# Kernel optimization log

Measured on AMD Instinct MI355X. Metric: run time of the kernel, lower is better.

## Reference

```python
import jax, jax.numpy as jnp
import numpy as np

BIT_WIDTH = 1
LEVELS = 2 ** BIT_WIDTH - 1
# Floyd-Steinberg gather weights (mirrored scatter kernel): contributions to
# pixel (r,c) from (r-1,c-1), (r-1,c), (r-1,c+1), (r,c-1)
W_UL, W_U, W_UR, W_L = 1.0 / 16, 5.0 / 16, 3.0 / 16, 7.0 / 16


def quant(x):
    return jnp.round(x * LEVELS) / LEVELS


def dither(x01):
    """Raster-scan error-diffusion dithering. x01: [B,C,R,W] in [0,1]."""
    B, C, R, W = x01.shape
    dtype = x01.dtype

    def row_step(prev_err, row_x):
        # prev_err: [B,C,W+2] zero-padded errors of previous row
        # row_x:    [W,B,C]   input values of current row
        up = (W_UL * prev_err[..., 0:W]
              + W_U * prev_err[..., 1:W + 1]
              + W_UR * prev_err[..., 2:W + 2])          # [B,C,W]
        up = jnp.moveaxis(up, -1, 0)                     # [W,B,C]

        def col_step(left_err, xs):
            x, u = xs                                    # each [B,C]
            val = jnp.clip(x + u + W_L * left_err, 0.0, 1.0)
            err = val - quant(val)
            return err, (val, err)

        _, (vals, errs) = jax.lax.scan(col_step, jnp.zeros((B, C), dtype), (row_x, up))
        err_row = jnp.pad(jnp.moveaxis(errs, 0, -1), ((0, 0), (0, 0), (1, 1)))  # [B,C,W+2]
        return err_row, jnp.moveaxis(vals, 0, -1)        # carry, [B,C,W]

    rows_x = jnp.moveaxis(jnp.moveaxis(x01, 2, 0), -1, 1)  # [R,W,B,C]
    init = jnp.zeros((B, C, W + 2), dtype)
    _, out_rows = jax.lax.scan(row_step, init, rows_x)      # [R,B,C,W]
    out = jnp.moveaxis(out_rows, 0, 2)                      # [B,C,R,W]
    return quant(out)


def setup_inputs() -> dict:
    key = jax.random.key(0)
    x = jax.random.normal(key, (32, 3, 512, 512), dtype=jnp.float32)
    return {"x": x}


def reference(x):
    x = jnp.clip(x, -1.0, 1.0)
    x01 = (x + 1.0) / 2.0
    y = dither(x01)
    return y * 2.0 - 1.0
```

## Files before the change

### kernel.cpp

```cpp
#include <hip/hip_runtime.h>


#define F_UL 0.0625f
#define F_U  0.3125f
#define F_UR 0.1875f
#define F_L  0.4375f

constexpr int WW    = 512;
constexpr int IMG   = WW * WW;
constexpr int NIMG  = 96;
constexpr int NW    = 8;
constexpr int BUFW  = 792;
constexpr int NCH   = 40;
constexpr int LAG   = 10;
constexpr int PPAIR = 320;
constexpr size_t XP_FLOATS = (size_t)NIMG * NW * PPAIR * 128;
constexpr size_t XP_BYTES  = XP_FLOATS * 4;
constexpr size_t XP_SLACK  = 8192;
constexpr size_t XP_OFF    = 4u * 1024 * 1024;
constexpr size_t WS_NEED   = XP_OFF + XP_BYTES + XP_SLACK;

__device__ __forceinline__ float wave_shr1(float v, float fill) {
  int r = __builtin_amdgcn_update_dpp(__float_as_int(fill), __float_as_int(v),
                                      0x138 , 0xF, 0xF, false);
  return __int_as_float(r);
}

__device__ __forceinline__ float pp(float xv) {
#pragma clang fp contract(off)
  float xc = fminf(fmaxf(xv, -1.0f), 1.0f);
  return (xc + 1.0f) * 0.5f;
}

__global__ __launch_bounds__(256)
void pack_kernel(const float* __restrict__ xin, float* __restrict__ xp) {
  __shared__ float tile[64 * 65];
  const int img = blockIdx.x, w = blockIdx.y, ct = blockIdx.z;
  const int C   = ct * 64;
  const int tid = threadIdx.x;

  const float* xg = xin + (size_t)img * IMG + (size_t)w * 64 * WW;
  for (int k = 0; k < 4; ++k) {
    int flat = tid + 256 * k;
    int row = flat >> 4, cq = flat & 15;
    float4 v = *(const float4*)(xg + row * WW + C + cq * 4);
    float* d = tile + row * 65 + cq * 4;
    d[0] = pp(v.x); d[1] = pp(v.y); d[2] = pp(v.z); d[3] = pp(v.w);
  }
  __syncthreads();

  float* ob = xp + ((size_t)(img * NW + w) * PPAIR + 32 * ct) * 128;
  const int l = tid & 63, mo = tid >> 6;
  const int kst = (l - mo + 3) >> 2;
  for (int k = 0; k < 8; ++k) {
    int m = mo + 4 * (kst + k);
    if (m <= 94) {
      int c = 2 * (m - l);
      float2 v = make_float2(tile[l * 65 + c], tile[l * 65 + c + 1]);
      *(float2*)(ob + (size_t)m * 128 + 2 * l) = v;
    }
  }
}

__global__ __launch_bounds__(512, 1)
void dither_packed(const float* __restrict__ xp, uint2* __restrict__ yb) {
  __shared__ float bnd[(NW + 1) * BUFW];
  __shared__ int flags[NW];

  const int  tid  = threadIdx.x;
  const int  wave = tid >> 6;
  const int  lane = tid & 63;
  const int  img  = blockIdx.x;
  const bool l63  = (lane == 63);

  for (int i = tid; i < (NW + 1) * BUFW; i += 512) bnd[i] = 0.0f;
  if (tid < NW) flags[tid] = 0;
  __syncthreads();

  uint2* ybw = yb + (size_t)(img * NW + wave) * (10 * 64);
  const float* xw = xp + ((size_t)(img * NW + wave) * PPAIR) * 128 + lane * 2;
  float* bufR = bnd + wave * BUFW;
  float* bufW = bnd + (wave + 1) * BUFW;
  const int c0 = -2 * lane;

  float2 A0 = *(const float2*)(xw + 0 * 128);
  float2 A1 = *(const float2*)(xw + 1 * 128);
  float2 A2 = *(const float2*)(xw + 2 * 128);
  float2 A3 = *(const float2*)(xw + 3 * 128);
  float2 m0 = *(const float2*)(xw + 4 * 128);
  float2 m1 = *(const float2*)(xw + 5 * 128);
  float2 m2 = *(const float2*)(xw + 6 * 128);
  float2 m3 = *(const float2*)(xw + 7 * 128);
  float2 f0 = *(const float2*)(xw + 8 * 128);
  float2 f1 = *(const float2*)(xw + 9 * 128);
  float2 f2 = *(const float2*)(xw + 10 * 128);
  float2 f3 = *(const float2*)(xw + 11 * 128);
  float2 g0 = *(const float2*)(xw + 12 * 128);
  float2 g1 = *(const float2*)(xw + 13 * 128);
  float2 g2 = *(const float2*)(xw + 14 * 128);
  float2 g3 = *(const float2*)(xw + 15 * 128);
  float xq0 = A0.x, xq1 = A0.y, xq2 = A1.x, xq3 = A1.y;
  float xq4 = A2.x, xq5 = A2.y, xq6 = A3.x, xq7 = A3.y;

  if (wave) {
    while (__hip_atomic_load(&flags[wave - 1], __ATOMIC_RELAXED,
                             __HIP_MEMORY_SCOPE_WORKGROUP) < LAG)
      __builtin_amdgcn_s_sleep(1);
    __asm__ volatile("s_waitcnt lgkmcnt(0)" ::: "memory");
  }

  float err = 0.0f, s2 = 0.0f;
  float s1 = (lane == 0) ? bufR[129] : 0.0f;
  float2 qa = *(const float2*)(bufR + 130);
  float2 qb = *(const float2*)(bufR + 132);
  float2 qc = *(const float2*)(bufR + 134);
  float2 qd = *(const float2*)(bufR + 136);
  float2 fa = *(const float2*)(bufR + 138);
  float2 fb = *(const float2*)(bufR + 140);
  float2 fc = *(const float2*)(bufR + 142);
  float2 fd = *(const float2*)(bufR + 144);

  unsigned accLo = 0u, accHi = 0u;

  auto step = [&](int c, float qv, float xv) -> float {
#pragma clang fp contract(off)
    float e_in = wave_shr1(err, qv);
    float t1   = F_UL * s2;
    float t2   = F_U  * s1;
    float t3   = F_UR * e_in;
    float u    = (t1 + t2) + t3;
    float a1   = xv + u;
    float b    = F_L * err;
    float v    = a1 + b;
    float val  = fminf(fmaxf(v, 0.0f), 1.0f);
    float qn   = rintf(val);
    float e    = val - qn;
    float en   = ((unsigned)c < 512u) ? e : 0.0f;
    err = en; s2 = s1; s1 = e_in;
    return qn;
  };

  auto iter8 = [&](int T, unsigned& acc) {
    const int cg  = c0 + T;
    const int bsh = T & 31;
    const float* lp = xw + (size_t)(T / 2 + 16) * 128;
    float2 n0 = *(const float2*)(lp + 0 * 128);
    float2 n1 = *(const float2*)(lp + 1 * 128);
    float2 n2 = *(const float2*)(lp + 2 * 128);
    float2 n3 = *(const float2*)(lp + 3 * 128);
    float2 h0 = *(const float2*)(bufR + (T + 146));
    float2 h1 = *(const float2*)(bufR + (T + 148));
    float2 h2 = *(const float2*)(bufR + (T + 150));
    float2 h3 = *(const float2*)(bufR + (T + 152));

    float p0 = step(cg + 0, qa.x, xq0); float e0 = err;
    float p1 = step(cg + 1, qa.y, xq1); float e1 = err;
    float p2 = step(cg + 2, qb.x, xq2); float e2 = err;
    float p3 = step(cg + 3, qb.y, xq3); float e3 = err;
    float p4 = step(cg + 4, qc.x, xq4); float e4 = err;
    float p5 = step(cg + 5, qc.y, xq5); float e5 = err;
    float p6 = step(cg + 6, qd.x, xq6); float e6 = err;
    float p7 = step(cg + 7, qd.y, xq7); float e7 = err;

    acc |= ((__float_as_uint(p0) >> 29) & 1u) << (bsh + 0);
    acc |= ((__float_as_uint(p1) >> 29) & 1u) << (bsh + 1);
    acc |= ((__float_as_uint(p2) >> 29) & 1u) << (bsh + 2);
    acc |= ((__float_as_uint(p3) >> 29) & 1u) << (bsh + 3);
    acc |= ((__float_as_uint(p4) >> 29) & 1u) << (bsh + 4);
    acc |= ((__float_as_uint(p5) >> 29) & 1u) << (bsh + 5);
    acc |= ((__float_as_uint(p6) >> 29) & 1u) << (bsh + 6);
    acc |= ((__float_as_uint(p7) >> 29) & 1u) << (bsh + 7);

    if (l63) {
      float* bw = bufW + (cg + 129);
      bw[0] = e0; bw[1] = e1; bw[2] = e2; bw[3] = e3;
      bw[4] = e4; bw[5] = e5; bw[6] = e6; bw[7] = e7;
    }

    xq0 = m0.x; xq1 = m0.y; xq2 = m1.x; xq3 = m1.y;
    xq4 = m2.x; xq5 = m2.y; xq6 = m3.x; xq7 = m3.y;
    m0 = f0; m1 = f1; m2 = f2; m3 = f3;
    f0 = g0; f1 = g1; f2 = g2; f3 = g3;
    g0 = n0; g1 = n1; g2 = n2; g3 = n3;
    qa = fa; qb = fb; qc = fc; qd = fd;
    fa = h0; fb = h1; fc = h2; fd = h3;
  };

  for (int j = 0; j < NCH; ++j) {
    if (wave) {
      int need = j + LAG; if (need > NCH) need = NCH;
      while (__hip_atomic_load(&flags[wave - 1], __ATOMIC_RELAXED,
                               __HIP_MEMORY_SCOPE_WORKGROUP) < need)
        __builtin_amdgcn_s_sleep(1);
      __asm__ volatile("s_waitcnt lgkmcnt(0)" ::: "memory");
    }
    if (j & 2) { iter8(16 * j, accHi); iter8(16 * j + 8, accHi); }
    else       { iter8(16 * j, accLo); iter8(16 * j + 8, accLo); }
    if ((j & 3) == 3) {
      ybw[(j >> 2) * 64 + lane] = make_uint2(accLo, accHi);
      accLo = 0u; accHi = 0u;
    }
    if (l63) {
      __asm__ volatile("s_waitcnt lgkmcnt(0)" ::: "memory");
      __hip_atomic_store(&flags[wave], j + 1, __ATOMIC_RELAXED,
                         __HIP_MEMORY_SCOPE_WORKGROUP);
    }
  }
}

__global__ __launch_bounds__(256)
void unpack_kernel(const unsigned long long* __restrict__ yb,
                   float* __restrict__ yout) {
  const int img = blockIdx.x, w = blockIdx.y;
  const int wv = threadIdx.x >> 6, lane = threadIdx.x & 63;
  const unsigned long long* ybr = yb + (size_t)(img * NW + w) * 640;
  float* yb0 = yout + (size_t)img * IMG + (size_t)w * 64 * WW;

  for (int rr = 0; rr < 16; ++rr) {
    const int r  = wv * 16 + rr;
    const int t0 = 8 * lane + 2 * r;
    const int t64 = t0 >> 6, sh = t0 & 63;
    unsigned long long w1 = ybr[(size_t)t64 * 64 + r];
    unsigned long long w2 = ybr[(size_t)(t64 + 1) * 64 + r];
    unsigned bits = (unsigned)((w1 >> sh) | ((w2 << 1) << (63 - sh)));
    float* orow = yb0 + (size_t)r * WW + 8 * lane;
    float4 v0, v1;
    v0.x = (bits & 1u)   ? 1.0f : -1.0f;
    v0.y = (bits & 2u)   ? 1.0f : -1.0f;
    v0.z = (bits & 4u)   ? 1.0f : -1.0f;
    v0.w = (bits & 8u)   ? 1.0f : -1.0f;
    v1.x = (bits & 16u)  ? 1.0f : -1.0f;
    v1.y = (bits & 32u)  ? 1.0f : -1.0f;
    v1.z = (bits & 64u)  ? 1.0f : -1.0f;
    v1.w = (bits & 128u) ? 1.0f : -1.0f;
    *(float4*)(orow)     = v0;
    *(float4*)(orow + 4) = v1;
  }
}

__global__ __launch_bounds__(512, 1)
void dither_direct(const float* __restrict__ xin, float* __restrict__ yout) {
  __shared__ float bnd[(NW + 1) * BUFW];
  __shared__ int flags[NW];

  const int  tid  = threadIdx.x;
  const int  wave = tid >> 6;
  const int  lane = tid & 63;
  const int  img  = blockIdx.x;
  const bool l63  = (lane == 63);

  for (int i = tid; i < (NW + 1) * BUFW; i += 512) bnd[i] = 0.0f;
  if (tid < NW) flags[tid] = 0;
  __syncthreads();

  const int r = wave * 64 + lane;
  const float* xrow = xin + (size_t)img * IMG + (size_t)r * WW;
  float*       yrow = yout + (size_t)img * IMG + (size_t)r * WW;
  float* bufR = bnd + wave * BUFW;
  float* bufW = bnd + (wave + 1) * BUFW;
  const int c0 = -2 * lane;

  auto ldx = [&](int c) -> float2 { return *(const float2*)(xrow + (c & 511)); };

  float2 A0 = ldx(c0 + 0),  A1 = ldx(c0 + 2),  A2 = ldx(c0 + 4),  A3 = ldx(c0 + 6);
  float2 pB0 = ldx(c0 + 8),  pB1 = ldx(c0 + 10), pB2 = ldx(c0 + 12), pB3 = ldx(c0 + 14);
  float2 pC0 = ldx(c0 + 16), pC1 = ldx(c0 + 18), pC2 = ldx(c0 + 20), pC3 = ldx(c0 + 22);
  float xq0 = pp(A0.x), xq1 = pp(A0.y), xq2 = pp(A1.x), xq3 = pp(A1.y);
  float xq4 = pp(A2.x), xq5 = pp(A2.y), xq6 = pp(A3.x), xq7 = pp(A3.y);
  float2 pA0 = pB0, pA1 = pB1, pA2 = pB2, pA3 = pB3;
  pB0 = pC0; pB1 = pC1; pB2 = pC2; pB3 = pC3;

  if (wave) {
    while (__hip_atomic_load(&flags[wave - 1], __ATOMIC_RELAXED,
                             __HIP_MEMORY_SCOPE_WORKGROUP) < LAG)
      __builtin_amdgcn_s_sleep(1);
    __asm__ volatile("s_waitcnt lgkmcnt(0)" ::: "memory");
  }

  float err = 0.0f, s2 = 0.0f;
  float s1 = (lane == 0) ? bufR[129] : 0.0f;
  float2 qa = *(const float2*)(bufR + 130);
  float2 qb = *(const float2*)(bufR + 132);
  float2 qc = *(const float2*)(bufR + 134);
  float2 qd = *(const float2*)(bufR + 136);
  float2 fa = *(const float2*)(bufR + 138);
  float2 fb = *(const float2*)(bufR + 140);
  float2 fc = *(const float2*)(bufR + 142);
  float2 fd = *(const float2*)(bufR + 144);

  auto step = [&](int c, float qv, float xv) -> float {
#pragma clang fp contract(off)
    float e_in = wave_shr1(err, qv);
    float t1   = F_UL * s2;
    float t2   = F_U  * s1;
    float t3   = F_UR * e_in;
    float u    = (t1 + t2) + t3;
    float a1   = xv + u;
    float b    = F_L * err;
    float v    = a1 + b;
    float val  = fminf(fmaxf(v, 0.0f), 1.0f);
    float qn   = rintf(val);
    float e    = val - qn;
    float en   = ((unsigned)c < 512u) ? e : 0.0f;
    err = en; s2 = s1; s1 = e_in;
    return __builtin_fmaf(qn, 2.0f, -1.0f);
  };

  auto iter8 = [&](int T) {
    const int cg = c0 + T;
    float2 n0 = ldx(cg + 24), n1 = ldx(cg + 26), n2 = ldx(cg + 28), n3 = ldx(cg + 30);
    float2 h0 = *(const float2*)(bufR + (T + 146));
    float2 h1 = *(const float2*)(bufR + (T + 148));
    float2 h2 = *(const float2*)(bufR + (T + 150));
    float2 h3 = *(const float2*)(bufR + (T + 152));
    float w0 = pp(pA0.x), w1 = pp(pA0.y), w2 = pp(pA1.x), w3 = pp(pA1.y);
    float w4 = pp(pA2.x), w5 = pp(pA2.y), w6 = pp(pA3.x), w7 = pp(pA3.y);

    float y0 = step(cg + 0, qa.x, xq0); float e0 = err;
    float y1 = step(cg + 1, qa.y, xq1); float e1 = err;
    float y2 = step(cg + 2, qb.x, xq2); float e2 = err;
    float y3 = step(cg + 3, qb.y, xq3); float e3 = err;
    float y4 = step(cg + 4, qc.x, xq4); float e4 = err;
    float y5 = step(cg + 5, qc.y, xq5); float e5 = err;
    float y6 = step(cg + 6, qd.x, xq6); float e6 = err;
    float y7 = step(cg + 7, qd.y, xq7); float e7 = err;

    if ((unsigned)(cg + 0) < 511u) *(float2*)(yrow + cg + 0) = make_float2(y0, y1);
    if ((unsigned)(cg + 2) < 511u) *(float2*)(yrow + cg + 2) = make_float2(y2, y3);
    if ((unsigned)(cg + 4) < 511u) *(float2*)(yrow + cg + 4) = make_float2(y4, y5);
    if ((unsigned)(cg + 6) < 511u) *(float2*)(yrow + cg + 6) = make_float2(y6, y7);

    if (l63) {
      float* bw = bufW + (cg + 129);
      bw[0] = e0; bw[1] = e1; bw[2] = e2; bw[3] = e3;
      bw[4] = e4; bw[5] = e5; bw[6] = e6; bw[7] = e7;
    }

    xq0 = w0; xq1 = w1; xq2 = w2; xq3 = w3;
    xq4 = w4; xq5 = w5; xq6 = w6; xq7 = w7;
    pA0 = pB0; pA1 = pB1; pA2 = pB2; pA3 = pB3;
    pB0 = n0;  pB1 = n1;  pB2 = n2;  pB3 = n3;
    qa = fa; qb = fb; qc = fc; qd = fd;
    fa = h0; fb = h1; fc = h2; fd = h3;
  };

  for (int j = 0; j < NCH; ++j) {
    if (wave) {
      int need = j + LAG; if (need > NCH) need = NCH;
      while (__hip_atomic_load(&flags[wave - 1], __ATOMIC_RELAXED,
                               __HIP_MEMORY_SCOPE_WORKGROUP) < need)
        __builtin_amdgcn_s_sleep(1);
      __asm__ volatile("s_waitcnt lgkmcnt(0)" ::: "memory");
    }
    iter8(16 * j);
    iter8(16 * j + 8);
    if (l63) {
      __asm__ volatile("s_waitcnt lgkmcnt(0)" ::: "memory");
      __hip_atomic_store(&flags[wave], j + 1, __ATOMIC_RELAXED,
                         __HIP_MEMORY_SCOPE_WORKGROUP);
    }
  }
}

extern "C" void kernel_launch(void* const* d_in, const int* in_sizes, int n_in,
                              void* d_out, int out_size, void* d_ws, size_t ws_size,
                              hipStream_t stream) {
  const float* x = (const float*)d_in[0];
  float*       y = (float*)d_out;
  if (ws_size >= WS_NEED) {
    unsigned long long* yb = (unsigned long long*)d_ws;
    float* xp = (float*)((char*)d_ws + XP_OFF);
    pack_kernel<<<dim3(NIMG, NW, 8), dim3(256), 0, stream>>>(x, xp);
    dither_packed<<<dim3(NIMG), dim3(512), 0, stream>>>(xp, (uint2*)yb);
    unpack_kernel<<<dim3(NIMG, NW), dim3(256), 0, stream>>>(yb, y);
  } else {
    dither_direct<<<dim3(NIMG), dim3(512), 0, stream>>>(x, y);
  }
}
```

Before: 328.7 us.

## Pad out-of-range pixels with sentinel in pack, drop column bounds check in dither

The pack kernel now runs one block per image strip and walks column tiles through a 4-deep shared ring. It writes a -8 sentinel for out-of-range diagonal positions, so the dither step clamps these to zero error and can drop its per-step column bounds select. The dither loop is unrolled by four chunks with rotating register arrays, which replaces the long register shift chains. It also caches the last-seen flag value to skip redundant LDS polls and uses fmed3 for the clamp. The risks are less parallelism in pack (a smaller grid with serialized tiles) and a correctness dependence on the sentinel producing exactly zero error.

Result: faster. 282.6 us (-14.0%).

```diff
diff --git a/kernel.cpp b/kernel.cpp
--- a/kernel.cpp
+++ b/kernel.cpp
@@ -34,31 +34,44 @@
 
 __global__ __launch_bounds__(256)
 void pack_kernel(const float* __restrict__ xin, float* __restrict__ xp) {
-  __shared__ float tile[64 * 65];
-  const int img = blockIdx.x, w = blockIdx.y, ct = blockIdx.z;
-  const int C   = ct * 64;
+  __shared__ float ring[4 * 4160];
+  const int img = blockIdx.x, w = blockIdx.y;
   const int tid = threadIdx.x;
+  const int wv  = tid >> 6, l = tid & 63;
 
   const float* xg = xin + (size_t)img * IMG + (size_t)w * 64 * WW;
-  for (int k = 0; k < 4; ++k) {
-    int flat = tid + 256 * k;
-    int row = flat >> 4, cq = flat & 15;
-    float4 v = *(const float4*)(xg + row * WW + C + cq * 4);
-    float* d = tile + row * 65 + cq * 4;
-    d[0] = pp(v.x); d[1] = pp(v.y); d[2] = pp(v.z); d[3] = pp(v.w);
-  }
+  float* ob = xp + ((size_t)(img * NW + w) * PPAIR) * 128;
+
+  auto load_tile = [&](int t) {
+    float* dst = ring + (t & 3) * 4160;
+    const float* src = xg + 64 * t;
+#pragma unroll
+    for (int k = 0; k < 4; ++k) {
+      int flat = tid + 256 * k;
+      int row = flat >> 4, cq = flat & 15;
+      float4 v = *(const float4*)(src + row * WW + cq * 4);
+      float* d = dst + row * 65 + cq * 4;
+      d[0] = pp(v.x); d[1] = pp(v.y); d[2] = pp(v.z); d[3] = pp(v.w);
+    }
+  };
+
+  load_tile(0);
   __syncthreads();
-
-  float* ob = xp + ((size_t)(img * NW + w) * PPAIR + 32 * ct) * 128;
-  const int l = tid & 63, mo = tid >> 6;
-  const int kst = (l - mo + 3) >> 2;
-  for (int k = 0; k < 8; ++k) {
-    int m = mo + 4 * (kst + k);
-    if (m <= 94) {
-      int c = 2 * (m - l);
-      float2 v = make_float2(tile[l * 65 + c], tile[l * 65 + c + 1]);
-      *(float2*)(ob + (size_t)m * 128 + 2 * l) = v;
-    }
+  for (int t = 0; t < 10; ++t) {
+    if (t < 7) load_tile(t + 1);
+    const int Mb = 32 * t + 8 * wv;
+#pragma unroll
+    for (int i = 0; i < 8; ++i) {
+      const int M  = Mb + i;
+      const int g  = 2 * (M - l);
+      const int gm = g & 511;
+      const int idx = ((gm >> 6) & 3) * 4160 + l * 65 + (gm & 63);
+      const bool ok = ((unsigned)g < 512u);
+      float va = ring[idx], vb = ring[idx + 1];
+      float2 v = make_float2(ok ? va : -8.0f, ok ? vb : -8.0f);
+      *(float2*)(ob + (size_t)M * 128 + 2 * l) = v;
+    }
+    __syncthreads();
   }
 }
 
@@ -81,48 +94,36 @@
   const float* xw = xp + ((size_t)(img * NW + wave) * PPAIR) * 128 + lane * 2;
   float* bufR = bnd + wave * BUFW;
   float* bufW = bnd + (wave + 1) * BUFW;
-  const int c0 = -2 * lane;
-
-  float2 A0 = *(const float2*)(xw + 0 * 128);
-  float2 A1 = *(const float2*)(xw + 1 * 128);
-  float2 A2 = *(const float2*)(xw + 2 * 128);
-  float2 A3 = *(const float2*)(xw + 3 * 128);
-  float2 m0 = *(const float2*)(xw + 4 * 128);
-  float2 m1 = *(const float2*)(xw + 5 * 128);
-  float2 m2 = *(const float2*)(xw + 6 * 128);
-  float2 m3 = *(const float2*)(xw + 7 * 128);
-  float2 f0 = *(const float2*)(xw + 8 * 128);
-  float2 f1 = *(const float2*)(xw + 9 * 128);
-  float2 f2 = *(const float2*)(xw + 10 * 128);
-  float2 f3 = *(const float2*)(xw + 11 * 128);
-  float2 g0 = *(const float2*)(xw + 12 * 128);
-  float2 g1 = *(const float2*)(xw + 13 * 128);
-  float2 g2 = *(const float2*)(xw + 14 * 128);
-  float2 g3 = *(const float2*)(xw + 15 * 128);
-  float xq0 = A0.x, xq1 = A0.y, xq2 = A1.x, xq3 = A1.y;
-  float xq4 = A2.x, xq5 = A2.y, xq6 = A3.x, xq7 = A3.y;
-
+
+  float2 X0[4], X1[4], X2[4], X3[4], X4[4], X5[4], X6[4], X7[4];
+#pragma unroll
+  for (int i = 0; i < 4; ++i) {
+    X0[i] = *(const float2*)(xw + (size_t)(0  + i) * 128);
+    X1[i] = *(const float2*)(xw + (size_t)(4  + i) * 128);
+    X2[i] = *(const float2*)(xw + (size_t)(8  + i) * 128);
+    X3[i] = *(const float2*)(xw + (size_t)(12 + i) * 128);
+  }
+
+  int seen = 0;
   if (wave) {
-    while (__hip_atomic_load(&flags[wave - 1], __ATOMIC_RELAXED,
-                             __HIP_MEMORY_SCOPE_WORKGROUP) < LAG)
+    while ((seen = __hip_atomic_load(&flags[wave - 1], __ATOMIC_RELAXED,
+                                     __HIP_MEMORY_SCOPE_WORKGROUP)) < LAG)
       __builtin_amdgcn_s_sleep(1);
     __asm__ volatile("s_waitcnt lgkmcnt(0)" ::: "memory");
   }
 
   float err = 0.0f, s2 = 0.0f;
   float s1 = (lane == 0) ? bufR[129] : 0.0f;
-  float2 qa = *(const float2*)(bufR + 130);
-  float2 qb = *(const float2*)(bufR + 132);
-  float2 qc = *(const float2*)(bufR + 134);
-  float2 qd = *(const float2*)(bufR + 136);
-  float2 fa = *(const float2*)(bufR + 138);
-  float2 fb = *(const float2*)(bufR + 140);
-  float2 fc = *(const float2*)(bufR + 142);
-  float2 fd = *(const float2*)(bufR + 144);
+  float2 Q0[4], Q1[4];
+#pragma unroll
+  for (int i = 0; i < 4; ++i) {
+    Q0[i] = *(const float2*)(bufR + 130 + 2 * i);
+    Q1[i] = *(const float2*)(bufR + 138 + 2 * i);
+  }
 
   unsigned accLo = 0u, accHi = 0u;
 
-  auto step = [&](int c, float qv, float xv) -> float {
+  auto step = [&](float qv, float xv) -> float {
 #pragma clang fp contract(off)
     float e_in = wave_shr1(err, qv);
     float t1   = F_UL * s2;
@@ -132,35 +133,34 @@
     float a1   = xv + u;
     float b    = F_L * err;
     float v    = a1 + b;
-    float val  = fminf(fmaxf(v, 0.0f), 1.0f);
+    float val  = __builtin_amdgcn_fmed3f(v, 0.0f, 1.0f);
     float qn   = rintf(val);
-    float e    = val - qn;
-    float en   = ((unsigned)c < 512u) ? e : 0.0f;
-    err = en; s2 = s1; s1 = e_in;
+    err = val - qn;
+    s2 = s1; s1 = e_in;
     return qn;
   };
 
-  auto iter8 = [&](int T, unsigned& acc) {
-    const int cg  = c0 + T;
-    const int bsh = T & 31;
+  auto iter8 = [&](float2 (&XC)[4], float2 (&XL)[4], float2 (&QC)[4],
+                   int T, int bsh, unsigned& acc) {
     const float* lp = xw + (size_t)(T / 2 + 16) * 128;
-    float2 n0 = *(const float2*)(lp + 0 * 128);
-    float2 n1 = *(const float2*)(lp + 1 * 128);
-    float2 n2 = *(const float2*)(lp + 2 * 128);
-    float2 n3 = *(const float2*)(lp + 3 * 128);
-    float2 h0 = *(const float2*)(bufR + (T + 146));
-    float2 h1 = *(const float2*)(bufR + (T + 148));
-    float2 h2 = *(const float2*)(bufR + (T + 150));
-    float2 h3 = *(const float2*)(bufR + (T + 152));
-
-    float p0 = step(cg + 0, qa.x, xq0); float e0 = err;
-    float p1 = step(cg + 1, qa.y, xq1); float e1 = err;
-    float p2 = step(cg + 2, qb.x, xq2); float e2 = err;
-    float p3 = step(cg + 3, qb.y, xq3); float e3 = err;
-    float p4 = step(cg + 4, qc.x, xq4); float e4 = err;
-    float p5 = step(cg + 5, qc.y, xq5); float e5 = err;
-    float p6 = step(cg + 6, qd.x, xq6); float e6 = err;
-    float p7 = step(cg + 7, qd.y, xq7); float e7 = err;
+    XL[0] = *(const float2*)(lp + 0 * 128);
+    XL[1] = *(const float2*)(lp + 1 * 128);
+    XL[2] = *(const float2*)(lp + 2 * 128);
+    XL[3] = *(const float2*)(lp + 3 * 128);
+
+    float p0 = step(QC[0].x, XC[0].x); float e0 = err;
+    float p1 = step(QC[0].y, XC[0].y); float e1 = err;
+    float p2 = step(QC[1].x, XC[1].x); float e2 = err;
+    float p3 = step(QC[1].y, XC[1].y); float e3 = err;
+    float p4 = step(QC[2].x, XC[2].x); float e4 = err;
+    float p5 = step(QC[2].y, XC[2].y); float e5 = err;
+    float p6 = step(QC[3].x, XC[3].x); float e6 = err;
+    float p7 = step(QC[3].y, XC[3].y); float e7 = err;
+
+    QC[0] = *(const float2*)(bufR + (T + 146));
+    QC[1] = *(const float2*)(bufR + (T + 148));
+    QC[2] = *(const float2*)(bufR + (T + 150));
+    QC[3] = *(const float2*)(bufR + (T + 152));
 
     acc |= ((__float_as_uint(p0) >> 29) & 1u) << (bsh + 0);
     acc |= ((__float_as_uint(p1) >> 29) & 1u) << (bsh + 1);
@@ -172,39 +172,51 @@
     acc |= ((__float_as_uint(p7) >> 29) & 1u) << (bsh + 7);
 
     if (l63) {
-      float* bw = bufW + (cg + 129);
+      float* bw = bufW + (T + 3);
       bw[0] = e0; bw[1] = e1; bw[2] = e2; bw[3] = e3;
       bw[4] = e4; bw[5] = e5; bw[6] = e6; bw[7] = e7;
     }
-
-    xq0 = m0.x; xq1 = m0.y; xq2 = m1.x; xq3 = m1.y;
-    xq4 = m2.x; xq5 = m2.y; xq6 = m3.x; xq7 = m3.y;
-    m0 = f0; m1 = f1; m2 = f2; m3 = f3;
-    f0 = g0; f1 = g1; f2 = g2; f3 = g3;
-    g0 = n0; g1 = n1; g2 = n2; g3 = n3;
-    qa = fa; qb = fb; qc = fc; qd = fd;
-    fa = h0; fb = h1; fc = h2; fd = h3;
-  };
-
-  for (int j = 0; j < NCH; ++j) {
+  };
+
+  auto waitflag = [&](int j) {
     if (wave) {
       int need = j + LAG; if (need > NCH) need = NCH;
-      while (__hip_atomic_load(&flags[wave - 1], __ATOMIC_RELAXED,
-                               __HIP_MEMORY_SCOPE_WORKGROUP) < need)
-        __builtin_amdgcn_s_sleep(1);
-      __asm__ volatile("s_waitcnt lgkmcnt(0)" ::: "memory");
-    }
-    if (j & 2) { iter8(16 * j, accHi); iter8(16 * j + 8, accHi); }
-    else       { iter8(16 * j, accLo); iter8(16 * j + 8, accLo); }
-    if ((j & 3) == 3) {
-      ybw[(j >> 2) * 64 + lane] = make_uint2(accLo, accHi);
-      accLo = 0u; accHi = 0u;
-    }
+      if (seen < need) {
+        while ((seen = __hip_atomic_load(&flags[wave - 1], __ATOMIC_RELAXED,
+                                         __HIP_MEMORY_SCOPE_WORKGROUP)) < need)
+          __builtin_amdgcn_s_sleep(1);
+        __asm__ volatile("s_waitcnt lgkmcnt(0)" ::: "memory");
+      }
+    }
+  };
+  auto pubflag = [&](int v) {
     if (l63) {
       __asm__ volatile("s_waitcnt lgkmcnt(0)" ::: "memory");
-      __hip_atomic_store(&flags[wave], j + 1, __ATOMIC_RELAXED,
+      __hip_atomic_store(&flags[wave], v, __ATOMIC_RELAXED,
                          __HIP_MEMORY_SCOPE_WORKGROUP);
     }
+  };
+
+  for (int jj = 0; jj < NCH; jj += 4) {
+    const int T0 = 16 * jj;
+    waitflag(jj);
+    iter8(X0, X4, Q0, T0 + 0,  0,  accLo);
+    iter8(X1, X5, Q1, T0 + 8,  8,  accLo);
+    pubflag(jj + 1);
+    waitflag(jj + 1);
+    iter8(X2, X6, Q0, T0 + 16, 16, accLo);
+    iter8(X3, X7, Q1, T0 + 24, 24, accLo);
+    pubflag(jj + 2);
+    waitflag(jj + 2);
+    iter8(X4, X0, Q0, T0 + 32, 0,  accHi);
+    iter8(X5, X1, Q1, T0 + 40, 8,  accHi);
+    pubflag(jj + 3);
+    waitflag(jj + 3);
+    iter8(X6, X2, Q0, T0 + 48, 16, accHi);
+    iter8(X7, X3, Q1, T0 + 56, 24, accHi);
+    pubflag(jj + 4);
+    ybw[(jj >> 2) * 64 + lane] = make_uint2(accLo, accHi);
+    accLo = 0u; accHi = 0u;
   }
 }
 
@@ -370,7 +382,7 @@
   if (ws_size >= WS_NEED) {
     unsigned long long* yb = (unsigned long long*)d_ws;
     float* xp = (float*)((char*)d_ws + XP_OFF);
-    pack_kernel<<<dim3(NIMG, NW, 8), dim3(256), 0, stream>>>(x, xp);
+    pack_kernel<<<dim3(NIMG, NW), dim3(256), 0, stream>>>(x, xp);
     dither_packed<<<dim3(NIMG), dim3(512), 0, stream>>>(xp, (uint2*)yb);
     unpack_kernel<<<dim3(NIMG, NW), dim3(256), 0, stream>>>(yb, y);
   } else {
```
